# Kernel tuning notes

Hardware: AMD Instinct MI355X
Metric: run time of the kernel (lower is better)

## Reference

```python
import jax, jax.numpy as jnp
import numpy as np

EPS = 1e-12  # matches torch F.normalize default eps
TEMPERATURE = 0.07

def _l2_normalize(x):
    norm = jnp.sqrt(jnp.sum(x * x, axis=-1, keepdims=True))
    return x / jnp.maximum(norm, EPS)

def setup_inputs() -> dict:
    key = jax.random.key(0)
    k1, k2 = jax.random.split(key)
    N, D = 4096, 1024
    z1 = jax.random.normal(k1, (N, D), dtype=jnp.float32)
    z2 = jax.random.normal(k2, (N, D), dtype=jnp.float32)
    return {"z1": z1, "z2": z2}

def reference(z1, z2):
    # L2-normalize both sets; cosine similarity of unit vectors is a dot product,
    # so the broadcast CosineSimilarity collapses to a single GEMM.
    z1n = _l2_normalize(z1)
    z2n = _l2_normalize(z2)
    logits = jnp.einsum('nd,md->nm', z1n, z2n) / TEMPERATURE  # [N, N]
    # CrossEntropyLoss with labels = arange(N): mean of -log_softmax diagonal.
    logp = jax.nn.log_softmax(logits, axis=-1)
    loss = -jnp.mean(jnp.diagonal(logp))
    return loss
```

## Files before the change

kernel.cpp:

```cpp
#include <hip/hip_runtime.h>

#define N_ROWS 4096
#define DIM 1024
#define INV_T (1.0f / 0.07f)
#define FP8_SCALE 16.0f
#define EXP_SCALE (INV_T * 1.44269504088896f / 256.0f)
#define BK 128
#define NJT 32

typedef __attribute__((ext_vector_type(4))) float floatx4;
typedef __attribute__((ext_vector_type(4))) int int4x;
typedef __attribute__((ext_vector_type(8))) int int8x;

__device__ inline unsigned int f2e4m3(float x) {
    unsigned int u = __float_as_uint(x);
    unsigned int s = (u >> 24) & 0x80u;
    int e = (int)((u >> 23) & 0xffu);
    unsigned int m = u & 0x7fffffu;
    if (e < 121) return s;
    unsigned int t = m >> 20;
    unsigned int rest = m & 0xFFFFFu;
    t += (rest > 0x80000u) || (rest == 0x80000u && (t & 1u));
    int e8 = e - 120;
    if (t == 8u) { t = 0u; e8 += 1; }
    return s | ((unsigned int)e8 << 3) | t;
}

__global__ __launch_bounds__(256) void k_normalize(
    const float* __restrict__ z1, const float* __restrict__ z2,
    unsigned char* __restrict__ z1f, unsigned char* __restrict__ z2f,
    float* __restrict__ diag, float* __restrict__ out) {
    const int lane = threadIdx.x & 63, wave = threadIdx.x >> 6;
    const int row = blockIdx.x * 4 + wave;

    if (blockIdx.x == 0 && threadIdx.x == 0) out[0] = 0.f;

    const float4* A = reinterpret_cast<const float4*>(z1 + (size_t)row * DIM);
    const float4* B = reinterpret_cast<const float4*>(z2 + (size_t)row * DIM);
    float4 a[4], b[4];
    #pragma unroll
    for (int rep = 0; rep < 4; ++rep) {
        a[rep] = A[lane + 64 * rep];
        b[rep] = B[lane + 64 * rep];
    }

    float s11 = 0.f, s22 = 0.f, s12 = 0.f;
    #pragma unroll
    for (int rep = 0; rep < 4; ++rep) {
        s11 += a[rep].x * a[rep].x + a[rep].y * a[rep].y
             + a[rep].z * a[rep].z + a[rep].w * a[rep].w;
        s22 += b[rep].x * b[rep].x + b[rep].y * b[rep].y
             + b[rep].z * b[rep].z + b[rep].w * b[rep].w;
        s12 += a[rep].x * b[rep].x + a[rep].y * b[rep].y
             + a[rep].z * b[rep].z + a[rep].w * b[rep].w;
    }
    #pragma unroll
    for (int m = 32; m >= 1; m >>= 1) {
        s11 += __shfl_xor(s11, m, 64);
        s22 += __shfl_xor(s22, m, 64);
        s12 += __shfl_xor(s12, m, 64);
    }

    const float n1 = fmaxf(sqrtf(s11), 1e-12f);
    const float n2 = fmaxf(sqrtf(s22), 1e-12f);
    if (lane == 0) diag[row] = s12 / (n1 * n2) * INV_T;
    const float i1 = FP8_SCALE / n1, i2 = FP8_SCALE / n2;

    unsigned int* O1 = reinterpret_cast<unsigned int*>(z1f + (size_t)row * DIM);
    unsigned int* O2 = reinterpret_cast<unsigned int*>(z2f + (size_t)row * DIM);
    #pragma unroll
    for (int rep = 0; rep < 4; ++rep) {
        unsigned int pa = f2e4m3(a[rep].x * i1) | (f2e4m3(a[rep].y * i1) << 8)
                        | (f2e4m3(a[rep].z * i1) << 16) | (f2e4m3(a[rep].w * i1) << 24);
        unsigned int pb = f2e4m3(b[rep].x * i2) | (f2e4m3(b[rep].y * i2) << 8)
                        | (f2e4m3(b[rep].z * i2) << 16) | (f2e4m3(b[rep].w * i2) << 24);
        O1[lane + 64 * rep] = pa;
        O2[lane + 64 * rep] = pb;
    }
}

__global__ __launch_bounds__(256) void k_gemm_sumexp(
    const unsigned char* __restrict__ z1f, const unsigned char* __restrict__ z2f,
    float* __restrict__ P) {
    __shared__ __attribute__((aligned(16))) unsigned char As[128 * BK];
    __shared__ __attribute__((aligned(16))) unsigned char Bs[128 * BK];

    const int iT = blockIdx.y, jT = blockIdx.x;
    const int lane = threadIdx.x & 63, wave = threadIdx.x >> 6;
    const int wm = wave >> 1, wn = wave & 1;
    const int ml = lane & 15, q = lane >> 4;
    const int i0 = iT * 128, j0 = jT * 128;

    const int srow = lane >> 3;
    const int sg = ((lane & 7) ^ (srow & 7)) * 16;

    const int rs = ml & 7;
    const int slotL = ((2 * q) ^ rs) * 16;
    const int slotH = ((2 * q + 1) ^ rs) * 16;

    floatx4 acc[4][4];
    #pragma unroll
    for (int mt = 0; mt < 4; ++mt)
        #pragma unroll
        for (int nt = 0; nt < 4; ++nt)
            acc[mt][nt] = (floatx4){0.f, 0.f, 0.f, 0.f};

    for (int k0 = 0; k0 < DIM; k0 += BK) {
        #pragma unroll
        for (int c = 0; c < 4; ++c) {
            const int issue = wave * 4 + c;
            const int row = issue * 8 + srow;
            const unsigned char* gA = z1f + (size_t)(i0 + row) * DIM + k0 + sg;
            const unsigned char* gB = z2f + (size_t)(j0 + row) * DIM + k0 + sg;
            __builtin_amdgcn_global_load_lds(
                (const __attribute__((address_space(1))) void*)gA,
                (__attribute__((address_space(3))) void*)(As + issue * 1024), 16, 0, 0);
            __builtin_amdgcn_global_load_lds(
                (const __attribute__((address_space(1))) void*)gB,
                (__attribute__((address_space(3))) void*)(Bs + issue * 1024), 16, 0, 0);
        }
        __syncthreads();

        int8x af[4], bf[4];
        #pragma unroll
        for (int t = 0; t < 4; ++t) {
            const unsigned char* rowA = As + (wm * 64 + t * 16 + ml) * BK;
            const unsigned char* rowB = Bs + (wn * 64 + t * 16 + ml) * BK;
            int4x aL = *reinterpret_cast<const int4x*>(rowA + slotL);
            int4x aH = *reinterpret_cast<const int4x*>(rowA + slotH);
            int4x bLo = *reinterpret_cast<const int4x*>(rowB + slotL);
            int4x bHi = *reinterpret_cast<const int4x*>(rowB + slotH);
            af[t] = __builtin_shufflevector(aL, aH, 0, 1, 2, 3, 4, 5, 6, 7);
            bf[t] = __builtin_shufflevector(bLo, bHi, 0, 1, 2, 3, 4, 5, 6, 7);
        }
        #pragma unroll
        for (int mt = 0; mt < 4; ++mt)
            #pragma unroll
            for (int nt = 0; nt < 4; ++nt)
                acc[mt][nt] = __builtin_amdgcn_mfma_scale_f32_16x16x128_f8f6f4(
                    af[mt], bf[nt], acc[mt][nt],
                    0 , 0 ,
                    0, 0x7F , 0, 0x7F );
        __syncthreads();
    }

    float vv[4][4];
    #pragma unroll
    for (int mt = 0; mt < 4; ++mt) {
        #pragma unroll
        for (int r = 0; r < 4; ++r) {
            float v = 0.f;
            #pragma unroll
            for (int nt = 0; nt < 4; ++nt)
                v += __builtin_amdgcn_exp2f(acc[mt][nt][r] * EXP_SCALE);
            v += __shfl_xor(v, 1, 64);
            v += __shfl_xor(v, 2, 64);
            v += __shfl_xor(v, 4, 64);
            v += __shfl_xor(v, 8, 64);
            vv[mt][r] = v;
        }
    }
    float* Pl = reinterpret_cast<float*>(As);
    if (wn == 1 && ml == 0) {
        #pragma unroll
        for (int mt = 0; mt < 4; ++mt)
            #pragma unroll
            for (int r = 0; r < 4; ++r)
                Pl[wm * 64 + mt * 16 + q * 4 + r] = vv[mt][r];
    }
    __syncthreads();
    if (wn == 0 && ml == 0) {
        #pragma unroll
        for (int mt = 0; mt < 4; ++mt)
            #pragma unroll
            for (int r = 0; r < 4; ++r) {
                const int ri = wm * 64 + mt * 16 + q * 4 + r;
                P[jT * N_ROWS + i0 + ri] = vv[mt][r] + Pl[ri];
            }
    }
}

__global__ __launch_bounds__(128) void k_finalize(
    const float* __restrict__ P, const float* __restrict__ diag,
    float* __restrict__ out) {
    const int t = threadIdx.x;
    const int i = blockIdx.x * 128 + t;
    float s = 0.f;
    #pragma unroll
    for (int jt = 0; jt < NJT; ++jt)
        s += P[jt * N_ROWS + i];
    float v = logf(s) - diag[i];
    #pragma unroll
    for (int m = 32; m >= 1; m >>= 1)
        v += __shfl_xor(v, m, 64);
    __shared__ float r[2];
    if ((t & 63) == 0) r[t >> 6] = v;
    __syncthreads();
    if (t == 0) atomicAdd(out, (r[0] + r[1]) * (1.0f / N_ROWS));
}

extern "C" void kernel_launch(void* const* d_in, const int* in_sizes, int n_in,
                              void* d_out, int out_size, void* d_ws, size_t ws_size,
                              hipStream_t stream) {
    const float* z1 = (const float*)d_in[0];
    const float* z2 = (const float*)d_in[1];

    char* ws = (char*)d_ws;
    unsigned char* z1f = (unsigned char*)ws;
    unsigned char* z2f = (unsigned char*)(ws + (size_t)N_ROWS * DIM);
    float* diag = (float*)(ws + (size_t)N_ROWS * DIM * 2);
    float* P = diag + N_ROWS;

    k_normalize<<<N_ROWS / 4, 256, 0, stream>>>(z1, z2, z1f, z2f, diag,
                                                (float*)d_out);
    k_gemm_sumexp<<<dim3(NJT, 32), 256, 0, stream>>>(z1f, z2f, P);
    k_finalize<<<32, 128, 0, stream>>>(P, diag, (float*)d_out);
}
```

Before: 104.4 us.

## Fuse finalize into GEMM epilogue via atomic row sums and last-block counter

Removes the separate finalize kernel. Each GEMM block now atomically adds its per-row partial sum-of-exp into a shared row-sum array, and a per-row-tile counter identifies the last block, which then computes log minus the diagonal and accumulates the loss. This saves one kernel launch and the partial-sum buffer round trip. In exchange it adds global float atomics, a completion counter and an extra barrier, and the floating-point summation order is no longer deterministic.

New measurement: 110.2 us. +5.6%, slower.

```diff
diff --git a/kernel.cpp b/kernel.cpp
--- a/kernel.cpp
+++ b/kernel.cpp
@@ -29,11 +29,15 @@
 __global__ __launch_bounds__(256) void k_normalize(
     const float* __restrict__ z1, const float* __restrict__ z2,
     unsigned char* __restrict__ z1f, unsigned char* __restrict__ z2f,
-    float* __restrict__ diag, float* __restrict__ out) {
+    float* __restrict__ diag, float* __restrict__ S,
+    unsigned int* __restrict__ ctr, float* __restrict__ out) {
     const int lane = threadIdx.x & 63, wave = threadIdx.x >> 6;
     const int row = blockIdx.x * 4 + wave;
 
-    if (blockIdx.x == 0 && threadIdx.x == 0) out[0] = 0.f;
+    if (blockIdx.x == 0) {
+        if (threadIdx.x < 32) ctr[threadIdx.x] = 0u;
+        else if (threadIdx.x == 32) out[0] = 0.f;
+    }
 
     const float4* A = reinterpret_cast<const float4*>(z1 + (size_t)row * DIM);
     const float4* B = reinterpret_cast<const float4*>(z2 + (size_t)row * DIM);
@@ -63,7 +67,10 @@
 
     const float n1 = fmaxf(sqrtf(s11), 1e-12f);
     const float n2 = fmaxf(sqrtf(s22), 1e-12f);
-    if (lane == 0) diag[row] = s12 / (n1 * n2) * INV_T;
+    if (lane == 0) {
+        diag[row] = s12 / (n1 * n2) * INV_T;
+        S[row] = 0.f;
+    }
     const float i1 = FP8_SCALE / n1, i2 = FP8_SCALE / n2;
 
     unsigned int* O1 = reinterpret_cast<unsigned int*>(z1f + (size_t)row * DIM);
@@ -81,9 +88,12 @@
 
 __global__ __launch_bounds__(256) void k_gemm_sumexp(
     const unsigned char* __restrict__ z1f, const unsigned char* __restrict__ z2f,
-    float* __restrict__ P) {
+    float* __restrict__ S, const float* __restrict__ diag,
+    unsigned int* __restrict__ ctr, float* __restrict__ out) {
     __shared__ __attribute__((aligned(16))) unsigned char As[128 * BK];
     __shared__ __attribute__((aligned(16))) unsigned char Bs[128 * BK];
+    __shared__ int sh_last;
+    __shared__ float rr[4];
 
     const int iT = blockIdx.y, jT = blockIdx.x;
     const int lane = threadIdx.x & 63, wave = threadIdx.x >> 6;
@@ -175,28 +185,33 @@
             #pragma unroll
             for (int r = 0; r < 4; ++r) {
                 const int ri = wm * 64 + mt * 16 + q * 4 + r;
-                P[jT * N_ROWS + i0 + ri] = vv[mt][r] + Pl[ri];
+                atomicAdd(&S[i0 + ri], vv[mt][r] + Pl[ri]);
             }
     }
-}
-
-__global__ __launch_bounds__(128) void k_finalize(
-    const float* __restrict__ P, const float* __restrict__ diag,
-    float* __restrict__ out) {
-    const int t = threadIdx.x;
-    const int i = blockIdx.x * 128 + t;
-    float s = 0.f;
-    #pragma unroll
-    for (int jt = 0; jt < NJT; ++jt)
-        s += P[jt * N_ROWS + i];
-    float v = logf(s) - diag[i];
-    #pragma unroll
-    for (int m = 32; m >= 1; m >>= 1)
-        v += __shfl_xor(v, m, 64);
-    __shared__ float r[2];
-    if ((t & 63) == 0) r[t >> 6] = v;
+
+    __builtin_amdgcn_s_waitcnt(0);
     __syncthreads();
-    if (t == 0) atomicAdd(out, (r[0] + r[1]) * (1.0f / N_ROWS));
+    if (threadIdx.x == 0) {
+        unsigned int old = atomicAdd(&ctr[iT], 1u);
+        sh_last = (old == NJT - 1);
+    }
+    __syncthreads();
+    if (sh_last) {
+        const int t = threadIdx.x;
+        float v = 0.f;
+        if (t < 128) {
+            float s = __hip_atomic_load(&S[i0 + t], __ATOMIC_RELAXED,
+                                        __HIP_MEMORY_SCOPE_AGENT);
+            v = logf(s) - diag[i0 + t];
+        }
+        #pragma unroll
+        for (int m = 32; m >= 1; m >>= 1)
+            v += __shfl_xor(v, m, 64);
+        if ((t & 63) == 0) rr[t >> 6] = v;
+        __syncthreads();
+        if (t == 0)
+            atomicAdd(out, (rr[0] + rr[1] + rr[2] + rr[3]) * (1.0f / N_ROWS));
+    }
 }
 
 extern "C" void kernel_launch(void* const* d_in, const int* in_sizes, int n_in,
@@ -209,10 +224,11 @@
     unsigned char* z1f = (unsigned char*)ws;
     unsigned char* z2f = (unsigned char*)(ws + (size_t)N_ROWS * DIM);
     float* diag = (float*)(ws + (size_t)N_ROWS * DIM * 2);
-    float* P = diag + N_ROWS;
-
-    k_normalize<<<N_ROWS / 4, 256, 0, stream>>>(z1, z2, z1f, z2f, diag,
+    float* S = diag + N_ROWS;
+    unsigned int* ctr = (unsigned int*)(S + N_ROWS);
+
+    k_normalize<<<N_ROWS / 4, 256, 0, stream>>>(z1, z2, z1f, z2f, diag, S, ctr,
                                                 (float*)d_out);
-    k_gemm_sumexp<<<dim3(NJT, 32), 256, 0, stream>>>(z1f, z2f, P);
-    k_finalize<<<32, 128, 0, stream>>>(P, diag, (float*)d_out);
-}
+    k_gemm_sumexp<<<dim3(NJT, 32), 256, 0, stream>>>(z1f, z2f, S, diag, ctr,
+                                                     (float*)d_out);
+}
```
